# Kernel optimization log

Hardware: AMD Instinct MI355X
Metric: run time of the kernel (lower is better)

The kernel has to match this reference:

```python
import jax, jax.numpy as jnp
import numpy as np

B, CIN, H, W = 32, 192, 56, 56
COUT, K, PAD, STRIDE = 192, 3, 1, 1


def setup_inputs() -> dict:
    key = jax.random.key(0)
    k1, k2 = jax.random.split(key, 2)
    x = jax.random.normal(k1, (B, CIN, H, W), dtype=jnp.float32)
    # torch Linear: weight [out_feature, in_feature*k*k], bias [out_feature]
    weight = jax.random.normal(k2, (COUT, CIN * K * K), dtype=jnp.float32) * 0.02
    bias = jnp.zeros((COUT,), dtype=jnp.float32)
    return {"x": x, "weight": weight, "bias": bias}


def reference(x, weight, bias):
    # pad H/W with zeros (F.pad constant)
    xp = jnp.pad(x, ((0, 0), (0, 0), (PAD, PAD), (PAD, PAD)))
    Bn, C, Hp, Wp = xp.shape
    Ho = (Hp - K) // STRIDE + 1
    Wo = (Wp - K) // STRIDE + 1
    # im2col matching torch.nn.Unfold layout: feature index = c*K*K + i*K + j
    # small fixed loop over K*K kernel offsets (9 slices), fully vectorized over B,C,Ho,Wo
    patches = jnp.stack(
        [xp[:, :, i : i + Ho * STRIDE : STRIDE, j : j + Wo * STRIDE : STRIDE]
         for i in range(K) for j in range(K)],
        axis=2,
    )  # [B, C, K*K, Ho, Wo]
    cols = patches.reshape(Bn, C * K * K, Ho * Wo)  # [B, C*K*K, L]
    # Linear over transposed unfold: out[b, l, o] = cols[b, :, l] @ weight[o, :].T + bias
    out = jnp.einsum('bkl,ok->bol', cols, weight) + bias[None, :, None]
    # rearrange 'b (h w) c -> b c h w' with h=w=sqrt(L)
    return out.reshape(Bn, COUT, Ho, Wo)
```

## Files before the change

kernel.cpp:

```cpp
#include <hip/hip_runtime.h>

typedef __attribute__((ext_vector_type(8))) short short8;
typedef __attribute__((ext_vector_type(4))) float floatx4;

#define CIN    192
#define COUTN  192
#define HWDIM  56
#define HWSZ   (56*56)
#define KWT    1728
#define TH     4
#define HY     6
#define PH     58
#define CK     32
#define NCHUNK 6
#define MT     64

#define XPACK_SHORTS (32u*6u*58u*58u*32u)
#define WPACK_SHORTS (3u*6u*9u*64u*32u)
#define WS_NEEDED    ((size_t)(XPACK_SHORTS + WPACK_SHORTS) * 2u)

__device__ __forceinline__ short f2bf(float f) {
    union { float f; unsigned u; } v; v.f = f;
    unsigned u = v.u + 0x7FFFu + ((v.u >> 16) & 1u);
    return (short)(u >> 16);
}

__device__ __forceinline__ unsigned pk2(float lo, float hi) {
    union { float f; unsigned u; } a, b;
    a.f = lo; b.f = hi;
    unsigned ua = a.u + 0x7FFFu + ((a.u >> 16) & 1u);
    unsigned ub = b.u + 0x7FFFu + ((b.u >> 16) & 1u);
    return (ua >> 16) | (ub & 0xFFFF0000u);
}

#define XP_P 788

__global__ __launch_bounds__(256)
void pack_x(const float* __restrict__ x, short* __restrict__ xp) {
    __shared__ unsigned sp[16 * XP_P];
    const int tid = threadIdx.x;
    const int bid = blockIdx.x;
    const int rg  = bid & 3;
    const int cc  = (bid >> 2) % 6;
    const int b   = bid / 24;
    const int h0  = rg * 14;

    const float* base = x + ((size_t)(b * CIN + cc * 32) * HWSZ + (size_t)h0 * HWDIM);
    for (int i = tid; i < 16 * 196; i += 256) {
        int a = i / 196;
        int j = i - a * 196;
        const float4 f0 = *(const float4*)(base + (size_t)(2 * a)     * HWSZ + j * 4);
        const float4 f1 = *(const float4*)(base + (size_t)(2 * a + 1) * HWSZ + j * 4);
        uint4 u;
        u.x = pk2(f0.x, f1.x);
        u.y = pk2(f0.y, f1.y);
        u.z = pk2(f0.z, f1.z);
        u.w = pk2(f0.w, f1.w);
        *(uint4*)&sp[a * XP_P + j * 4] = u;
    }
    __syncthreads();

    short* orow = xp + (((size_t)(b * 6 + cc) * PH + (h0 + 1)) * PH) * CK;
    for (int i = tid; i < 14 * 58 * 4; i += 256) {
        int g  = i & 3;
        int t  = i >> 2;
        int xq = t % 58;
        int r  = t / 58;
        uint4 u = (uint4){0u, 0u, 0u, 0u};
        if (xq > 0 && xq < 57) {
            int w = r * 56 + xq - 1;
            u.x = sp[(4 * g + 0) * XP_P + w];
            u.y = sp[(4 * g + 1) * XP_P + w];
            u.z = sp[(4 * g + 2) * XP_P + w];
            u.w = sp[(4 * g + 3) * XP_P + w];
        }
        int P = (h0 + 1 + r) * PH + xq;
        int s = g ^ ((P >> 1) & 3);
        *(uint4*)(orow + ((size_t)r * PH + xq) * CK + s * 8) = u;
    }

    if (rg == 0 || rg == 3) {
        int hq = (rg == 0) ? 0 : 57;
        short* prow = xp + (((size_t)(b * 6 + cc) * PH + hq) * PH) * CK;
        for (int i = tid; i < 58 * 4; i += 256)
            *(uint4*)(prow + (size_t)i * 8) = (uint4){0u, 0u, 0u, 0u};
    }
}

__global__ __launch_bounds__(256)
void pack_w(const float* __restrict__ w, short* __restrict__ wp) {
    int idx = blockIdx.x * 256 + threadIdx.x;
    const int TOT = 3 * 6 * 9 * 64 * 4;
    if (idx >= TOT) return;
    int cg = idx & 3;
    int m  = (idx >> 2) & 63;
    int t  = idx >> 8;
    int off = t % 9;  t /= 9;
    int cc  = t % 6;
    int og  = t / 6;
    short8 v;
#pragma unroll
    for (int k = 0; k < 8; ++k)
        v[k] = f2bf(w[(size_t)(og * 64 + m) * KWT + (cc * 32 + cg * 8 + k) * 9 + off]);
    *(short8*)(wp + (size_t)idx * 8) = v;
}

__global__ __launch_bounds__(256, 2)
void conv_main(const short* __restrict__ xp, const short* __restrict__ wp,
               const float* __restrict__ bias, float* __restrict__ out) {
    __shared__ __align__(16) short sh[HY * PH * CK];

    const int tid  = threadIdx.x;
    const int u    = blockIdx.x;
    const int xcd  = u & 7;
    const int slot = u >> 3;
    const int og   = slot % 3;
    const int tile = xcd * 56 + slot / 3;
    const int bx   = tile % 14;
    const int bb   = tile / 14;
    const int gh0  = bx * TH;
    const int lane = tid & 63;
    const int wave = tid >> 6;
    const int wm   = wave >> 1;
    const int wn   = wave & 1;
    const int g    = lane >> 4;
    const int col  = lane & 15;

    int ly[7], lx[7], pnt[7];
#pragma unroll
    for (int nt = 0; nt < 7; ++nt) {
        int l = wn * 112 + nt * 16 + col;
        ly[nt] = l / 56;
        lx[nt] = l % 56;
        pnt[nt] = ly[nt] * PH + lx[nt];
    }

    floatx4 acc[2][7];
#pragma unroll
    for (int mt = 0; mt < 2; ++mt)
#pragma unroll
        for (int nt = 0; nt < 7; ++nt)
            acc[mt][nt] = (floatx4){0.f, 0.f, 0.f, 0.f};

    const short8* wpk = (const short8*)wp;
    const int wlbase = wave * 64;

    for (int cc = 0; cc < NCHUNK; ++cc) {
        if (cc) __syncthreads();

        const short* src = xp + ((size_t)(bb * 6 + cc) * (PH * PH) + (size_t)gh0 * PH) * CK;
#pragma unroll
        for (int j = 0; j < 6; ++j) {
            int idx = j * 256 + tid;
            if (idx < HY * PH * 4) {
                __builtin_amdgcn_global_load_lds(
                    (const __attribute__((address_space(1))) void*)(src + (size_t)idx * 8),
                    (__attribute__((address_space(3))) void*)(sh + (j * 256 + wlbase) * 8),
                    16, 0, 0);
            }
        }

        short8 afr[9][2];
#pragma unroll
        for (int off = 0; off < 9; ++off)
#pragma unroll
            for (int mt = 0; mt < 2; ++mt)
                afr[off][mt] = wpk[((og * 6 + cc) * 9 + off) * 256 + (wm * 32 + mt * 16 + col) * 4 + g];

        __syncthreads();

#pragma unroll
        for (int off = 0; off < 9; ++off) {
            const int doff = (off / 3) * PH + (off % 3);
#pragma unroll
            for (int nt = 0; nt < 7; ++nt) {
                int p = pnt[nt] + doff;
                int s = ((p >> 1) & 3) ^ g;
                short8 bfr = *(const short8*)&sh[(p << 5) + (s << 3)];
                acc[0][nt] = __builtin_amdgcn_mfma_f32_16x16x32_bf16(afr[off][0], bfr, acc[0][nt], 0, 0, 0);
                acc[1][nt] = __builtin_amdgcn_mfma_f32_16x16x32_bf16(afr[off][1], bfr, acc[1][nt], 0, 0, 0);
            }
        }
    }

#pragma unroll
    for (int mt = 0; mt < 2; ++mt) {
        int o = og * 64 + wm * 32 + mt * 16 + g * 4;
#pragma unroll
        for (int nt = 0; nt < 7; ++nt) {
            int l  = wn * 112 + nt * 16 + col;
            int h  = gh0 + l / 56;
            int ww = l % 56;
            size_t base = ((size_t)(bb * COUTN + o) * HWDIM + h) * HWDIM + ww;
            floatx4 v = acc[mt][nt];
#pragma unroll
            for (int r2 = 0; r2 < 4; ++r2)
                out[base + (size_t)r2 * HWSZ] = v[r2] + bias[o + r2];
        }
    }
}

__global__ __launch_bounds__(256, 2)
void conv3x3_fb(const float* __restrict__ x, const float* __restrict__ w,
                const float* __restrict__ bias, float* __restrict__ out) {
    __shared__ __align__(16) short sh_halo[HY * PH * CK];
    __shared__ __align__(16) short sh_w[9 * MT * CK];
    const int tid = threadIdx.x;
    const int gh0 = blockIdx.x * TH;
    const int o0  = blockIdx.y * MT;
    const int bb  = blockIdx.z;
    const int lane = tid & 63, wave = tid >> 6;
    const int wm = wave >> 1, wn = wave & 1;
    const int g = lane >> 4, col = lane & 15;
    int ly[7], lx[7];
#pragma unroll
    for (int nt = 0; nt < 7; ++nt) {
        int l = wn * 112 + nt * 16 + col;
        ly[nt] = l / 56; lx[nt] = l % 56;
    }
    floatx4 acc[2][7];
#pragma unroll
    for (int mt = 0; mt < 2; ++mt)
#pragma unroll
        for (int nt = 0; nt < 7; ++nt) acc[mt][nt] = (floatx4){0.f,0.f,0.f,0.f};
    for (int cc = 0; cc < NCHUNK; ++cc) {
        const int c0 = cc * CK;
        if (cc) __syncthreads();
        for (int i = tid; i < 4 * HY * PH; i += 256) {
            int xx = i % PH, r = i / PH, y = r % HY, cg = r / HY;
            int gh = gh0 + y - 1, gw = xx - 1;
            bool ok = ((unsigned)gh < 56u) & ((unsigned)gw < 56u);
            const float* src = x + ((size_t)(bb * CIN + c0 + cg * 8) * HWDIM + gh) * HWDIM + gw;
            short8 v;
#pragma unroll
            for (int k = 0; k < 8; ++k) v[k] = f2bf(ok ? src[k * HWSZ] : 0.f);
            *(short8*)&sh_halo[(y * PH + xx) * CK + ((cg ^ ((xx >> 1) & 3)) << 3)] = v;
        }
        for (int i = tid; i < 9 * MT * 4; i += 256) {
            int cg = i & 3, off = (i >> 2) % 9, m = i / 36;
            const float* src = w + (size_t)(o0 + m) * KWT + (c0 + cg * 8) * 9 + off;
            short8 v;
#pragma unroll
            for (int k = 0; k < 8; ++k) v[k] = f2bf(src[k * 9]);
            *(short8*)&sh_w[(off * MT + m) * CK + ((cg ^ ((m >> 1) & 3)) << 3)] = v;
        }
        __syncthreads();
#pragma unroll
        for (int off = 0; off < 9; ++off) {
            const int di = off / 3, dj = off % 3;
            short8 a[2];
#pragma unroll
            for (int mt = 0; mt < 2; ++mt) {
                int m = wm * 32 + mt * 16 + col;
                a[mt] = *(const short8*)&sh_w[(off * MT + m) * CK + ((g ^ ((m >> 1) & 3)) << 3)];
            }
#pragma unroll
            for (int nt = 0; nt < 7; ++nt) {
                int yy = ly[nt] + di, xpp = lx[nt] + dj;
                short8 bfr = *(const short8*)&sh_halo[(yy * PH + xpp) * CK + ((g ^ ((xpp >> 1) & 3)) << 3)];
                acc[0][nt] = __builtin_amdgcn_mfma_f32_16x16x32_bf16(a[0], bfr, acc[0][nt], 0, 0, 0);
                acc[1][nt] = __builtin_amdgcn_mfma_f32_16x16x32_bf16(a[1], bfr, acc[1][nt], 0, 0, 0);
            }
        }
    }
#pragma unroll
    for (int mt = 0; mt < 2; ++mt) {
        int o = o0 + wm * 32 + mt * 16 + g * 4;
#pragma unroll
        for (int nt = 0; nt < 7; ++nt) {
            int l = wn * 112 + nt * 16 + col;
            int h = gh0 + l / 56, ww = l % 56;
            size_t base = ((size_t)(bb * COUTN + o) * HWDIM + h) * HWDIM + ww;
            floatx4 v = acc[mt][nt];
#pragma unroll
            for (int r2 = 0; r2 < 4; ++r2)
                out[base + (size_t)r2 * HWSZ] = v[r2] + bias[o + r2];
        }
    }
}

extern "C" void kernel_launch(void* const* d_in, const int* in_sizes, int n_in,
                              void* d_out, int out_size, void* d_ws, size_t ws_size,
                              hipStream_t stream) {
    const float* x  = (const float*)d_in[0];
    const float* wt = (const float*)d_in[1];
    const float* bi = (const float*)d_in[2];
    float* out = (float*)d_out;

    if (ws_size >= WS_NEEDED) {
        short* xpk = (short*)d_ws;
        short* wpk = xpk + XPACK_SHORTS;
        pack_x<<<32 * 6 * 4, 256, 0, stream>>>(x, xpk);
        {
            int tot = 3 * 6 * 9 * 64 * 4;
            pack_w<<<(tot + 255) / 256, 256, 0, stream>>>(wt, wpk);
        }
        conv_main<<<dim3(14 * 3 * 32), dim3(256), 0, stream>>>(xpk, wpk, bi, out);
    } else {
        conv3x3_fb<<<dim3(14, 3, 32), dim3(256), 0, stream>>>(x, wt, bi, out);
    }
}
```

Baseline: 207.4 us.

## Double-buffer halo staging, enlarge row tile, merge pack kernels

The conv kernel now processes 8 output rows per block with 512 threads (8 waves) and stages each channel chunk's halo into a second LDS buffer while the current chunk is being computed. This hides global-to-LDS load latency and cuts the count of halo re-reads, since a 10-row halo now covers 8 rows instead of a 6-row halo for 4. The x and w packing kernels are fused into one launch to save a kernel launch. The cost is more LDS per block (two 10-row buffers), higher register pressure under the 512-thread launch bound, and fewer blocks in total (672).

```diff
diff --git a/kernel.cpp b/kernel.cpp
--- a/kernel.cpp
+++ b/kernel.cpp
@@ -8,12 +8,13 @@
 #define HWDIM  56
 #define HWSZ   (56*56)
 #define KWT    1728
-#define TH     4
-#define HY     6
+#define TH     8
+#define HY     10
 #define PH     58
 #define CK     32
 #define NCHUNK 6
 #define MT     64
+#define HPC    (HY*PH*CK)
 
 #define XPACK_SHORTS (32u*6u*58u*58u*32u)
 #define WPACK_SHORTS (3u*6u*9u*64u*32u)
@@ -34,11 +35,33 @@
 }
 
 #define XP_P 788
+#define PXBLOCKS (32*6*4)
+#define PWTOT    (3*6*9*64*4)
 
 __global__ __launch_bounds__(256)
-void pack_x(const float* __restrict__ x, short* __restrict__ xp) {
+void pack_xw(const float* __restrict__ x, const float* __restrict__ w,
+             short* __restrict__ xp, short* __restrict__ wp) {
     __shared__ unsigned sp[16 * XP_P];
     const int tid = threadIdx.x;
+
+    if (blockIdx.x >= PXBLOCKS) {
+        int idx = (blockIdx.x - PXBLOCKS) * 256 + tid;
+        if (idx < PWTOT) {
+            int cg = idx & 3;
+            int m  = (idx >> 2) & 63;
+            int t  = idx >> 8;
+            int off = t % 9;  t /= 9;
+            int cc  = t % 6;
+            int og  = t / 6;
+            short8 v;
+#pragma unroll
+            for (int k = 0; k < 8; ++k)
+                v[k] = f2bf(w[(size_t)(og * 64 + m) * KWT + (cc * 32 + cg * 8 + k) * 9 + off]);
+            *(short8*)(wp + (size_t)idx * 8) = v;
+        }
+        return;
+    }
+
     const int bid = blockIdx.x;
     const int rg  = bid & 3;
     const int cc  = (bid >> 2) % 6;
@@ -68,11 +91,11 @@
         int r  = t / 58;
         uint4 u = (uint4){0u, 0u, 0u, 0u};
         if (xq > 0 && xq < 57) {
-            int w = r * 56 + xq - 1;
-            u.x = sp[(4 * g + 0) * XP_P + w];
-            u.y = sp[(4 * g + 1) * XP_P + w];
-            u.z = sp[(4 * g + 2) * XP_P + w];
-            u.w = sp[(4 * g + 3) * XP_P + w];
+            int wdx = r * 56 + xq - 1;
+            u.x = sp[(4 * g + 0) * XP_P + wdx];
+            u.y = sp[(4 * g + 1) * XP_P + wdx];
+            u.z = sp[(4 * g + 2) * XP_P + wdx];
+            u.w = sp[(4 * g + 3) * XP_P + wdx];
         }
         int P = (h0 + 1 + r) * PH + xq;
         int s = g ^ ((P >> 1) & 3);
@@ -87,52 +110,32 @@
     }
 }
 
-__global__ __launch_bounds__(256)
-void pack_w(const float* __restrict__ w, short* __restrict__ wp) {
-    int idx = blockIdx.x * 256 + threadIdx.x;
-    const int TOT = 3 * 6 * 9 * 64 * 4;
-    if (idx >= TOT) return;
-    int cg = idx & 3;
-    int m  = (idx >> 2) & 63;
-    int t  = idx >> 8;
-    int off = t % 9;  t /= 9;
-    int cc  = t % 6;
-    int og  = t / 6;
-    short8 v;
-#pragma unroll
-    for (int k = 0; k < 8; ++k)
-        v[k] = f2bf(w[(size_t)(og * 64 + m) * KWT + (cc * 32 + cg * 8 + k) * 9 + off]);
-    *(short8*)(wp + (size_t)idx * 8) = v;
-}
-
-__global__ __launch_bounds__(256, 2)
+__global__ __launch_bounds__(512, 4)
 void conv_main(const short* __restrict__ xp, const short* __restrict__ wp,
                const float* __restrict__ bias, float* __restrict__ out) {
-    __shared__ __align__(16) short sh[HY * PH * CK];
+    __shared__ __align__(16) short sh[2 * HPC];
 
     const int tid  = threadIdx.x;
     const int u    = blockIdx.x;
     const int xcd  = u & 7;
     const int slot = u >> 3;
     const int og   = slot % 3;
-    const int tile = xcd * 56 + slot / 3;
-    const int bx   = tile % 14;
-    const int bb   = tile / 14;
+    const int tile = xcd * 28 + slot / 3;
+    const int bx   = tile % 7;
+    const int bb   = tile / 7;
     const int gh0  = bx * TH;
     const int lane = tid & 63;
     const int wave = tid >> 6;
-    const int wm   = wave >> 1;
-    const int wn   = wave & 1;
+    const int wm   = wave >> 2;
+    const int wn   = wave & 3;
     const int g    = lane >> 4;
     const int col  = lane & 15;
 
-    int ly[7], lx[7], pnt[7];
+    int pnt[7];
 #pragma unroll
     for (int nt = 0; nt < 7; ++nt) {
         int l = wn * 112 + nt * 16 + col;
-        ly[nt] = l / 56;
-        lx[nt] = l % 56;
-        pnt[nt] = ly[nt] * PH + lx[nt];
+        pnt[nt] = (l / 56) * PH + (l % 56);
     }
 
     floatx4 acc[2][7];
@@ -144,30 +147,37 @@
 
     const short8* wpk = (const short8*)wp;
     const int wlbase = wave * 64;
+    const short* srcb = xp + ((size_t)bb * 6 * (PH * PH) + (size_t)gh0 * PH) * CK;
+
+#define STAGE(dstbuf, ccc)                                                              \
+    do {                                                                                \
+        const short* _src = srcb + (size_t)(ccc) * (PH * PH) * CK;                      \
+        short* _dst = sh + (dstbuf) * HPC;                                              \
+        _Pragma("unroll")                                                               \
+        for (int _j = 0; _j < 5; ++_j) {                                                \
+            int _idx = _j * 512 + tid;                                                  \
+            if (_idx < HY * PH * 4) {                                                   \
+                __builtin_amdgcn_global_load_lds(                                       \
+                    (const __attribute__((address_space(1))) void*)(_src + (size_t)_idx * 8), \
+                    (__attribute__((address_space(3))) void*)(_dst + (_j * 512 + wlbase) * 8), \
+                    16, 0, 0);                                                          \
+            }                                                                           \
+        }                                                                               \
+    } while (0)
+
+    short8 afr[9][2];
+    STAGE(0, 0);
+#pragma unroll
+    for (int off = 0; off < 9; ++off)
+#pragma unroll
+        for (int mt = 0; mt < 2; ++mt)
+            afr[off][mt] = wpk[((og * 6 + 0) * 9 + off) * 256 + (wm * 32 + mt * 16 + col) * 4 + g];
+    __syncthreads();
 
     for (int cc = 0; cc < NCHUNK; ++cc) {
-        if (cc) __syncthreads();
-
-        const short* src = xp + ((size_t)(bb * 6 + cc) * (PH * PH) + (size_t)gh0 * PH) * CK;
-#pragma unroll
-        for (int j = 0; j < 6; ++j) {
-            int idx = j * 256 + tid;
-            if (idx < HY * PH * 4) {
-                __builtin_amdgcn_global_load_lds(
-                    (const __attribute__((address_space(1))) void*)(src + (size_t)idx * 8),
-                    (__attribute__((address_space(3))) void*)(sh + (j * 256 + wlbase) * 8),
-                    16, 0, 0);
-            }
-        }
-
-        short8 afr[9][2];
-#pragma unroll
-        for (int off = 0; off < 9; ++off)
-#pragma unroll
-            for (int mt = 0; mt < 2; ++mt)
-                afr[off][mt] = wpk[((og * 6 + cc) * 9 + off) * 256 + (wm * 32 + mt * 16 + col) * 4 + g];
-
-        __syncthreads();
+        const short* cur = sh + (cc & 1) * HPC;
+
+        if (cc + 1 < NCHUNK) STAGE((cc + 1) & 1, cc + 1);
 
 #pragma unroll
         for (int off = 0; off < 9; ++off) {
@@ -176,12 +186,22 @@
             for (int nt = 0; nt < 7; ++nt) {
                 int p = pnt[nt] + doff;
                 int s = ((p >> 1) & 3) ^ g;
-                short8 bfr = *(const short8*)&sh[(p << 5) + (s << 3)];
+                short8 bfr = *(const short8*)&cur[(p << 5) + (s << 3)];
                 acc[0][nt] = __builtin_amdgcn_mfma_f32_16x16x32_bf16(afr[off][0], bfr, acc[0][nt], 0, 0, 0);
                 acc[1][nt] = __builtin_amdgcn_mfma_f32_16x16x32_bf16(afr[off][1], bfr, acc[1][nt], 0, 0, 0);
             }
         }
-    }
+
+        if (cc + 1 < NCHUNK) {
+#pragma unroll
+            for (int off = 0; off < 9; ++off)
+#pragma unroll
+                for (int mt = 0; mt < 2; ++mt)
+                    afr[off][mt] = wpk[((og * 6 + cc + 1) * 9 + off) * 256 + (wm * 32 + mt * 16 + col) * 4 + g];
+            __syncthreads();
+        }
+    }
+#undef STAGE
 
 #pragma unroll
     for (int mt = 0; mt < 2; ++mt) {
@@ -203,10 +223,10 @@
 __global__ __launch_bounds__(256, 2)
 void conv3x3_fb(const float* __restrict__ x, const float* __restrict__ w,
                 const float* __restrict__ bias, float* __restrict__ out) {
-    __shared__ __align__(16) short sh_halo[HY * PH * CK];
+    __shared__ __align__(16) short sh_halo[6 * PH * CK];
     __shared__ __align__(16) short sh_w[9 * MT * CK];
     const int tid = threadIdx.x;
-    const int gh0 = blockIdx.x * TH;
+    const int gh0 = blockIdx.x * 4;
     const int o0  = blockIdx.y * MT;
     const int bb  = blockIdx.z;
     const int lane = tid & 63, wave = tid >> 6;
@@ -226,8 +246,8 @@
     for (int cc = 0; cc < NCHUNK; ++cc) {
         const int c0 = cc * CK;
         if (cc) __syncthreads();
-        for (int i = tid; i < 4 * HY * PH; i += 256) {
-            int xx = i % PH, r = i / PH, y = r % HY, cg = r / HY;
+        for (int i = tid; i < 4 * 6 * PH; i += 256) {
+            int xx = i % PH, r = i / PH, y = r % 6, cg = r / 6;
             int gh = gh0 + y - 1, gw = xx - 1;
             bool ok = ((unsigned)gh < 56u) & ((unsigned)gw < 56u);
             const float* src = x + ((size_t)(bb * CIN + c0 + cg * 8) * HWDIM + gh) * HWDIM + gw;
@@ -290,12 +310,8 @@
     if (ws_size >= WS_NEEDED) {
         short* xpk = (short*)d_ws;
         short* wpk = xpk + XPACK_SHORTS;
-        pack_x<<<32 * 6 * 4, 256, 0, stream>>>(x, xpk);
-        {
-            int tot = 3 * 6 * 9 * 64 * 4;
-            pack_w<<<(tot + 255) / 256, 256, 0, stream>>>(wt, wpk);
-        }
-        conv_main<<<dim3(14 * 3 * 32), dim3(256), 0, stream>>>(xpk, wpk, bi, out);
+        pack_xw<<<PXBLOCKS + (PWTOT + 255) / 256, 256, 0, stream>>>(x, wt, xpk, wpk);
+        conv_main<<<dim3(672), dim3(512), 0, stream>>>(xpk, wpk, bi, out);
     } else {
         conv3x3_fb<<<dim3(14, 3, 32), dim3(256), 0, stream>>>(x, wt, bi, out);
     }
```

After: 524.3 us. +152.7%, slower.
